# Kernel tuning notes

Hardware: AMD Instinct MI355X
Metric: run time of the kernel (lower is better)

The kernel has to match this reference:

```python
import jax, jax.numpy as jnp
import numpy as np

H = 16          # num_attention_heads
SCALE = (1024.0 / 16.0) ** 0.5  # attention_head_size = hidden/num_hidden_layers
EPS = 1e-12
NEG = -jnp.inf


def layer_norm(x, g, b):
    mu = jnp.mean(x, axis=-1, keepdims=True)
    var = jnp.mean((x - mu) ** 2, axis=-1, keepdims=True)
    return (x - mu) * jax.lax.rsqrt(var + EPS) * g + b


def setup_inputs() -> dict:
    key = jax.random.key(0)
    ks = jax.random.split(key, 8)
    B, S, D, F = 4, 2048, 1024, 4096
    s = 0.02
    return {
        "hidden_state": jax.random.normal(ks[0], (B, S, D), jnp.float32),
        "attention_mask": jnp.ones((B, S), jnp.int32),
        "Wq": jax.random.normal(ks[1], (D, D), jnp.float32) * s,
        "Wk": jax.random.normal(ks[2], (D, D), jnp.float32) * s,
        "Wv": jax.random.normal(ks[3], (D, D), jnp.float32) * s,
        "Wo": jax.random.normal(ks[4], (D, D), jnp.float32) * s,
        "ln1_g": jnp.ones((D,), jnp.float32),
        "ln1_b": jnp.zeros((D,), jnp.float32),
        "W1": jax.random.normal(ks[5], (D, F), jnp.float32) * s,
        "b1": jnp.zeros((F,), jnp.float32),
        "W2": jax.random.normal(ks[6], (F, D), jnp.float32) * s,
        "b2": jnp.zeros((D,), jnp.float32),
        "ln2_g": jnp.ones((D,), jnp.float32),
        "ln2_b": jnp.zeros((D,), jnp.float32),
    }


def reference(hidden_state, attention_mask, Wq, Wk, Wv, Wo, ln1_g, ln1_b,
              W1, b1, W2, b2, ln2_g, ln2_b):
    B, S, D = hidden_state.shape
    # --- square attention mask (is_not_pad == 1) + causal ---
    amb = attention_mask == 1                              # [B,S] bool
    pair = amb[:, :, None] & amb[:, None, :]               # [B,S,S]
    self_mask = jnp.where(pair, 0.0, NEG)[:, None, :, :]   # [B,1,S,S]
    causal = jnp.where(jnp.triu(jnp.ones((S, S), bool), 1), NEG, 0.0)
    self_mask = self_mask + causal                         # [B,1,S,S]

    # --- self attention (pre-norm) ---
    residual = hidden_state
    x = layer_norm(hidden_state, ln1_g, ln1_b)
    q = (x @ Wq).reshape(B, S, H, D // H)
    k = (x @ Wk).reshape(B, S, H, D // H)
    v = (x @ Wv).reshape(B, S, H, D // H)
    scores = jnp.einsum('bqhd,bkhd->bhqk', q, k) / SCALE + self_mask
    probs = jax.nn.softmax(scores, axis=-1)                # dropout p=0
    ctx = jnp.einsum('bhqk,bkhd->bqhd', probs, v).reshape(B, S, D)
    x = ctx @ Wo + residual

    # --- feed forward (pre-norm, SiLU) ---
    residual = x
    y = layer_norm(x, ln2_g, ln2_b)
    y = jax.nn.silu(y @ W1 + b1) @ W2 + b2
    return y + residual
```

## Files before the change

### kernel.cpp

```cpp
#include <hip/hip_runtime.h>
#include <math.h>

typedef __attribute__((ext_vector_type(8))) short short8;
typedef __attribute__((ext_vector_type(4))) float floatx4;
typedef __attribute__((ext_vector_type(2))) unsigned int uintx2;

__device__ __forceinline__ float b2f(ushort u) {
    union { uint i; float f; } c; c.i = ((uint)u) << 16; return c.f;
}
__device__ __forceinline__ ushort f2b(float f) {
    union { float f; uint i; } c; c.f = f;
    return (ushort)((c.i + 0x7fffu + ((c.i >> 16) & 1u)) >> 16);
}

__device__ __forceinline__ void async_cp16(const ushort* g, ushort* l) {
    __builtin_amdgcn_global_load_lds(
        (const __attribute__((address_space(1))) void*)g,
        (__attribute__((address_space(3))) void*)l, 16, 0, 0);
}

__device__ __forceinline__ uint lds_u32(const void* p) {
    return (uint)(uintptr_t)(const __attribute__((address_space(3))) void*)p;
}

__device__ __forceinline__ float dpp_max16(float x) {
    int y;
    y = __builtin_amdgcn_update_dpp(__float_as_int(x), __float_as_int(x), 0xB1, 0xF, 0xF, false);
    x = fmaxf(x, __int_as_float(y));
    y = __builtin_amdgcn_update_dpp(__float_as_int(x), __float_as_int(x), 0x4E, 0xF, 0xF, false);
    x = fmaxf(x, __int_as_float(y));
    y = __builtin_amdgcn_update_dpp(__float_as_int(x), __float_as_int(x), 0x141, 0xF, 0xF, false);
    x = fmaxf(x, __int_as_float(y));
    y = __builtin_amdgcn_update_dpp(__float_as_int(x), __float_as_int(x), 0x140, 0xF, 0xF, false);
    x = fmaxf(x, __int_as_float(y));
    return x;
}

__global__ __launch_bounds__(256) void cvt_t_kernel(
    const float* __restrict__ S, ushort* __restrict__ D, int K, int N)
{
    __shared__ float ls[32][33];
    const int k0 = blockIdx.y * 32, n0 = blockIdx.x * 32;
    const int t = threadIdx.x;
    const int kr = t >> 3, nc = (t & 7) * 4;
    float4 f = *(const float4*)(S + (size_t)(k0 + kr) * N + n0 + nc);
    ls[kr][nc] = f.x; ls[kr][nc + 1] = f.y; ls[kr][nc + 2] = f.z; ls[kr][nc + 3] = f.w;
    __syncthreads();
    const int nr = t >> 3, kc = (t & 7) * 4;
    ushort4 o;
    o.x = f2b(ls[kc][nr]); o.y = f2b(ls[kc + 1][nr]);
    o.z = f2b(ls[kc + 2][nr]); o.w = f2b(ls[kc + 3][nr]);
    *(ushort4*)(D + (size_t)(n0 + nr) * K + k0 + kc) = o;
}

__global__ __launch_bounds__(256) void ln_kernel(
    const float* __restrict__ X, const float* __restrict__ G,
    const float* __restrict__ Bb, ushort* __restrict__ Y)
{
    const int row = blockIdx.x;
    const int t = threadIdx.x;
    const float* xr = X + (size_t)row * 1024;
    float4 p = ((const float4*)xr)[t];
    float s = p.x + p.y + p.z + p.w;
    float s2 = p.x * p.x + p.y * p.y + p.z * p.z + p.w * p.w;
    #pragma unroll
    for (int off = 32; off > 0; off >>= 1) {
        s += __shfl_down(s, off);
        s2 += __shfl_down(s2, off);
    }
    __shared__ float rs1[4], rs2[4];
    if ((t & 63) == 0) { rs1[t >> 6] = s; rs2[t >> 6] = s2; }
    __syncthreads();
    float S1 = rs1[0] + rs1[1] + rs1[2] + rs1[3];
    float S2 = rs2[0] + rs2[1] + rs2[2] + rs2[3];
    float mu = S1 * (1.0f / 1024.0f);
    float var = S2 * (1.0f / 1024.0f) - mu * mu;
    float rstd = rsqrtf(var + 1e-12f);
    float4 gp = ((const float4*)G)[t];
    float4 bp = ((const float4*)Bb)[t];
    ushort4 o;
    o.x = f2b((p.x - mu) * rstd * gp.x + bp.x);
    o.y = f2b((p.y - mu) * rstd * gp.y + bp.y);
    o.z = f2b((p.z - mu) * rstd * gp.z + bp.z);
    o.w = f2b((p.w - mu) * rstd * gp.w + bp.w);
    ((ushort4*)(Y + (size_t)row * 1024))[t] = o;
}

template<int BN, bool BIAS, bool SILU, bool RESID, bool OUTF32>
__global__ __launch_bounds__(256) void gemm_bt_kernel(
    const ushort* __restrict__ A, const ushort* __restrict__ Bt,
    const float* __restrict__ bias, const float* __restrict__ resid,
    void* __restrict__ Cm, int M, int N, int K)
{
    constexpr int NF = BN / 32;
    constexpr int BI = BN / 64;
    __shared__ __align__(16) ushort lsA[128 * 64];
    __shared__ __align__(16) ushort lsB[BN * 64];

    const int t = threadIdx.x;
    const int L = blockIdx.x + gridDim.x * blockIdx.y;
    const int cpx = (gridDim.x * gridDim.y) >> 3;
    const int wg = (L & 7) * cpx + (L >> 3);
    const int m0 = (wg / gridDim.x) * 128;
    const int n0 = (wg % gridDim.x) * BN;
    const int w = t >> 6;
    const int lane = t & 63;
    const int wm = (w >> 1) * 64;
    const int wn = (w & 1) * (BN / 2);
    const int quad = lane >> 4;
    const int l16 = lane & 15;

    const int lrow = lane >> 3;
    const int scol = ((lane & 7) ^ lrow) * 8;
    const ushort* gA = A + (size_t)(m0 + w * 32 + lrow) * K + scol;
    const ushort* gB = Bt + (size_t)(n0 + ((BI == 2) ? w * 32 : w * 16) + lrow) * K + scol;
    const int sw = l16 & 7;

    floatx4 acc[4][NF];
    #pragma unroll
    for (int i = 0; i < 4; ++i)
        #pragma unroll
        for (int j = 0; j < NF; ++j)
            acc[i][j] = (floatx4){0.f, 0.f, 0.f, 0.f};

    for (int k0 = 0; k0 < K; k0 += 64) {
        __syncthreads();
        #pragma unroll
        for (int i = 0; i < 4; ++i)
            async_cp16(gA + k0 + (size_t)(8 * i) * K, &lsA[(w * 32 + 8 * i) * 64]);
        if constexpr (BI == 2) {
            #pragma unroll
            for (int i = 0; i < 4; ++i)
                async_cp16(gB + k0 + (size_t)(8 * i) * K, &lsB[(w * 32 + 8 * i) * 64]);
        } else {
            #pragma unroll
            for (int i = 0; i < 2; ++i)
                async_cp16(gB + k0 + (size_t)(8 * i) * K, &lsB[(w * 16 + 8 * i) * 64]);
        }
        __syncthreads();

        #pragma unroll
        for (int h = 0; h < 2; ++h) {
            const int co = (((h << 2) | quad) ^ sw) * 8;
            short8 af[4], bf[NF];
            #pragma unroll
            for (int i = 0; i < 4; ++i)
                af[i] = *(const short8*)&lsA[(wm + i * 16 + l16) * 64 + co];
            #pragma unroll
            for (int j = 0; j < NF; ++j)
                bf[j] = *(const short8*)&lsB[(wn + j * 16 + l16) * 64 + co];
            #pragma unroll
            for (int i = 0; i < 4; ++i)
                #pragma unroll
                for (int j = 0; j < NF; ++j)
                    acc[i][j] = __builtin_amdgcn_mfma_f32_16x16x32_bf16(
                        af[i], bf[j], acc[i][j], 0, 0, 0);
        }
    }

    #pragma unroll
    for (int tn = 0; tn < NF; ++tn) {
        const int n = n0 + wn + tn * 16 + l16;
        const float bv = BIAS ? bias[n] : 0.0f;
        #pragma unroll
        for (int tm = 0; tm < 4; ++tm) {
            const int mbase = m0 + wm + tm * 16 + quad * 4;
            #pragma unroll
            for (int rr = 0; rr < 4; ++rr) {
                float v = acc[tm][tn][rr] + bv;
                if (SILU) v = v / (1.0f + __expf(-v));
                const size_t off = (size_t)(mbase + rr) * N + n;
                if (RESID) v += resid[off];
                if constexpr (OUTF32) ((float*)Cm)[off] = v;
                else                  ((ushort*)Cm)[off] = f2b(v);
            }
        }
    }
}

__global__ __launch_bounds__(256, 4) void attn_kernel(
    const ushort* __restrict__ Qm, const ushort* __restrict__ Km,
    const ushort* __restrict__ Vm, const int* __restrict__ amask,
    ushort* __restrict__ Om, int rs)
{
    __shared__ __align__(16) ushort lsQP[64][72];
    __shared__ __align__(16) ushort lsK[64][72];
    __shared__ __align__(16) ushort lsV2[2][4096];
    __shared__ int lsMk[64];

    const int L = blockIdx.x + (int)(gridDim.x * blockIdx.y);
    const int bh = L & 63;
    const int pr = L >> 6;
    const int b = bh >> 4, h = bh & 15;
    const int t = threadIdx.x;
    const int w = t >> 6, lane = t & 63;
    const int quad = lane >> 4, l16 = lane & 15;

    const size_t base = ((size_t)b * 2048) * rs + (size_t)h * 64;
    const size_t obase = ((size_t)b * 2048) * 1024 + (size_t)h * 64;

    const int krow = t >> 3, kc8 = (t & 7) << 3;
    const float scale2 = 0.125f * 1.44269504f;

    const int vkofs = ((lane >> 5) << 2) + ((lane >> 1) & 3);
    const int vdofs = ((lane >> 3) & 3) * 16 + (lane & 1) * 8;

    ushort* strip = &lsQP[w * 16][0];
    const uint strip_a = lds_u32(strip);
    char* wp_base = (char*)strip + l16 * 32 + quad * 8;
    const uint rp = strip_a + quad * 256 + l16 * 8;

    short8 ones8;
    #pragma unroll
    for (int i = 0; i < 8; ++i) ones8[i] = (short)0x3F80;

    #pragma unroll 1
    for (int half = 0; half < 2; ++half) {
        const int qt = half ? pr : (31 - pr);
        const int q0 = qt * 64;

        __syncthreads();

        async_cp16(Vm + base + (size_t)(16 * w + vkofs) * rs + vdofs,
                   &lsV2[0][(4 * w) * 256]);
        async_cp16(Vm + base + (size_t)(16 * w + 8 + vkofs) * rs + vdofs,
                   &lsV2[0][(4 * w + 2) * 256]);

        #pragma unroll
        for (int it = 0; it < 2; ++it) {
            int idx = it * 256 + t;
            int row = idx >> 3, c8 = (idx & 7) << 3;
            *(int4*)&lsQP[row][c8] =
                *(const int4*)(Qm + base + (size_t)(q0 + row) * rs + c8);
        }
        __syncthreads();

        short8 aq0 = *(const short8*)&lsQP[w * 16 + l16][quad * 8];
        short8 aq1 = *(const short8*)&lsQP[w * 16 + l16][32 + quad * 8];

        floatx4 Oacc[4];
        #pragma unroll
        for (int d = 0; d < 4; ++d) Oacc[d] = (floatx4){0.f, 0.f, 0.f, 0.f};
        floatx4 Lacc = (floatx4){0.f, 0.f, 0.f, 0.f};
        float m_i[4] = {-INFINITY, -INFINITY, -INFINITY, -INFINITY};

        int4 kr0 = *(const int4*)(Km + base + (size_t)krow * rs + kc8);
        int4 kr1 = *(const int4*)(Km + base + (size_t)(32 + krow) * rs + kc8);
        int mr = amask[b * 2048 + (t & 63)];

        for (int kt = 0; kt <= qt; ++kt) {
            __syncthreads();
            *(int4*)&lsK[krow][kc8] = kr0;
            *(int4*)&lsK[32 + krow][kc8] = kr1;
            if (t < 64) lsMk[t] = mr;
            __syncthreads();

            if (kt < qt) {
                const int kn = (kt + 1) * 64;
                kr0 = *(const int4*)(Km + base + (size_t)(kn + krow) * rs + kc8);
                kr1 = *(const int4*)(Km + base + (size_t)(kn + 32 + krow) * rs + kc8);
                mr = amask[b * 2048 + kn + (t & 63)];
                ushort* vd = &lsV2[(kt + 1) & 1][0];
                async_cp16(Vm + base + (size_t)(kn + 16 * w + vkofs) * rs + vdofs,
                           vd + (4 * w) * 256);
                async_cp16(Vm + base + (size_t)(kn + 16 * w + 8 + vkofs) * rs + vdofs,
                           vd + (4 * w + 2) * 256);
            }

            floatx4 sa[4];
            #pragma unroll
            for (int j = 0; j < 4; ++j) {
                short8 bk0 = *(const short8*)&lsK[j * 16 + l16][quad * 8];
                short8 bk1 = *(const short8*)&lsK[j * 16 + l16][32 + quad * 8];
                floatx4 z = (floatx4){0.f, 0.f, 0.f, 0.f};
                z = __builtin_amdgcn_mfma_f32_16x16x32_bf16(aq0, bk0, z, 0, 0, 0);
                sa[j] = __builtin_amdgcn_mfma_f32_16x16x32_bf16(aq1, bk1, z, 0, 0, 0);
            }

            float kb[4];
            #pragma unroll
            for (int j = 0; j < 4; ++j)
                kb[j] = (lsMk[j * 16 + l16] == 1) ? 0.f : -INFINITY;
            const bool diag = (kt == qt);

            float sv[4][4];
            float mxl[4];
            #pragma unroll
            for (int rr = 0; rr < 4; ++rr) {
                const int qrow = w * 16 + quad * 4 + rr;
                float mxv = -INFINITY;
                #pragma unroll
                for (int j = 0; j < 4; ++j) {
                    float v = sa[j][rr] * scale2 + kb[j];
                    if (diag) v = (j * 16 + l16 <= qrow) ? v : -INFINITY;
                    sv[rr][j] = v;
                    mxv = fmaxf(mxv, v);
                }
                mxl[rr] = mxv;
            }
            int grow = (mxl[0] > m_i[0] + 8.0f) | (mxl[1] > m_i[1] + 8.0f) |
                       (mxl[2] > m_i[2] + 8.0f) | (mxl[3] > m_i[3] + 8.0f);
            if (__any(grow)) {
                #pragma unroll
                for (int rr = 0; rr < 4; ++rr) {
                    const float mx = dpp_max16(mxl[rr]);
                    const float m_new = fmaxf(m_i[rr], mx);
                    const float al = exp2f(m_i[rr] - m_new);
                    m_i[rr] = m_new;
                    #pragma unroll
                    for (int d = 0; d < 4; ++d) Oacc[d][rr] *= al;
                    Lacc[rr] *= al;
                }
            }

            #pragma unroll
            for (int j = 0; j < 4; ++j) {
                float p0 = exp2f(sv[0][j] - m_i[0]);
                float p1 = exp2f(sv[1][j] - m_i[1]);
                float p2 = exp2f(sv[2][j] - m_i[2]);
                float p3 = exp2f(sv[3][j] - m_i[3]);
                uint w0, w1;
                asm("v_cvt_pk_bf16_f32 %0, %1, %2" : "=v"(w0) : "v"(p0), "v"(p1));
                asm("v_cvt_pk_bf16_f32 %0, %1, %2" : "=v"(w1) : "v"(p2), "v"(p3));
                *(uint2*)(wp_base + j * 512) = make_uint2(w0, w1);
            }

            asm volatile("s_waitcnt lgkmcnt(0)" ::: "memory");
            uintx2 t0, t1, t2, t3;
            asm volatile("ds_read_b64_tr_b16 %0, %1 offset:0"    : "=v"(t0) : "v"(rp));
            asm volatile("ds_read_b64_tr_b16 %0, %1 offset:128"  : "=v"(t1) : "v"(rp));
            asm volatile("ds_read_b64_tr_b16 %0, %1 offset:1024" : "=v"(t2) : "v"(rp));
            asm volatile("ds_read_b64_tr_b16 %0, %1 offset:1152" : "=v"(t3) : "v"(rp));
            asm volatile("s_waitcnt lgkmcnt(0)" ::: "memory");
            __builtin_amdgcn_sched_barrier(0);
            union { short8 s; uint u[4]; } ua0, ua1;
            ua0.u[0] = t0.x; ua0.u[1] = t0.y; ua0.u[2] = t1.x; ua0.u[3] = t1.y;
            ua1.u[0] = t2.x; ua1.u[1] = t2.y; ua1.u[2] = t3.x; ua1.u[3] = t3.y;
            const short8 ap0 = ua0.s;
            const short8 ap1 = ua1.s;

            const uint vb = lds_u32(&lsV2[kt & 1][0]) + quad * 1024 + l16 * 8;
            #pragma unroll
            for (int db = 0; db < 4; ++db) {
                const uint vbd = vb + db * 128;
                uintx2 v0, v1, v2, v3;
                asm volatile("ds_read_b64_tr_b16 %0, %1 offset:0"    : "=v"(v0) : "v"(vbd));
                asm volatile("ds_read_b64_tr_b16 %0, %1 offset:512"  : "=v"(v1) : "v"(vbd));
                asm volatile("ds_read_b64_tr_b16 %0, %1 offset:4096" : "=v"(v2) : "v"(vbd));
                asm volatile("ds_read_b64_tr_b16 %0, %1 offset:4608" : "=v"(v3) : "v"(vbd));
                asm volatile("s_waitcnt lgkmcnt(0)" ::: "memory");
                __builtin_amdgcn_sched_barrier(0);
                union { short8 s; uint u[4]; } ub0, ub1;
                ub0.u[0] = v0.x; ub0.u[1] = v0.y; ub0.u[2] = v1.x; ub0.u[3] = v1.y;
                ub1.u[0] = v2.x; ub1.u[1] = v2.y; ub1.u[2] = v3.x; ub1.u[3] = v3.y;
                Oacc[db] = __builtin_amdgcn_mfma_f32_16x16x32_bf16(ap0, ub0.s, Oacc[db], 0, 0, 0);
                Oacc[db] = __builtin_amdgcn_mfma_f32_16x16x32_bf16(ap1, ub1.s, Oacc[db], 0, 0, 0);
            }
            Lacc = __builtin_amdgcn_mfma_f32_16x16x32_bf16(ap0, ones8, Lacc, 0, 0, 0);
            Lacc = __builtin_amdgcn_mfma_f32_16x16x32_bf16(ap1, ones8, Lacc, 0, 0, 0);
        }

        #pragma unroll
        for (int rr = 0; rr < 4; ++rr) {
            const float inv = 1.0f / Lacc[rr];
            const int row = q0 + w * 16 + quad * 4 + rr;
            ushort* op = Om + obase + (size_t)row * 1024;
            #pragma unroll
            for (int d = 0; d < 4; ++d)
                op[d * 16 + l16] = f2b(Oacc[d][rr] * inv);
        }
    }
}

extern "C" void kernel_launch(void* const* d_in, const int* in_sizes, int n_in,
                              void* d_out, int out_size, void* d_ws, size_t ws_size,
                              hipStream_t stream) {
    const float* hidden = (const float*)d_in[0];
    const int*   amask  = (const int*)d_in[1];
    const float* Wq  = (const float*)d_in[2];
    const float* Wk  = (const float*)d_in[3];
    const float* Wv  = (const float*)d_in[4];
    const float* Wo  = (const float*)d_in[5];
    const float* l1g = (const float*)d_in[6];
    const float* l1b = (const float*)d_in[7];
    const float* W1  = (const float*)d_in[8];
    const float* b1  = (const float*)d_in[9];
    const float* W2  = (const float*)d_in[10];
    const float* b2  = (const float*)d_in[11];
    const float* l2g = (const float*)d_in[12];
    const float* l2b = (const float*)d_in[13];

    const int M = 8192;
    const size_t MB = 1048576;
    char* ws = (char*)d_ws;
    ushort* xa    = (ushort*)(ws);
    ushort* qkvb  = (ushort*)(ws + 16 * MB);
    ushort* Wqkvt = (ushort*)(ws + 64 * MB);
    ushort* Wot   = (ushort*)(ws + 70 * MB);
    ushort* W1t   = (ushort*)(ws);
    ushort* W2t   = (ushort*)(ws + 8 * MB);
    ushort* yb    = (ushort*)(ws + 16 * MB);
    ushort* hbc   = (ushort*)(ws + 32 * MB);
    float*  x2    = (float*)d_out;

    cvt_t_kernel<<<dim3(32, 32), 256, 0, stream>>>(Wq, Wqkvt, 1024, 1024);
    cvt_t_kernel<<<dim3(32, 32), 256, 0, stream>>>(Wk, Wqkvt + (size_t)1024 * 1024, 1024, 1024);
    cvt_t_kernel<<<dim3(32, 32), 256, 0, stream>>>(Wv, Wqkvt + (size_t)2048 * 1024, 1024, 1024);
    cvt_t_kernel<<<dim3(32, 32), 256, 0, stream>>>(Wo, Wot, 1024, 1024);

    ln_kernel<<<M, 256, 0, stream>>>(hidden, l1g, l1b, xa);
    gemm_bt_kernel<128, false, false, false, false><<<dim3(24, 64), 256, 0, stream>>>(
        xa, Wqkvt, nullptr, nullptr, qkvb, M, 3072, 1024);
    attn_kernel<<<dim3(16, 64), 256, 0, stream>>>(
        qkvb, qkvb + 1024, qkvb + 2048, amask, xa, 3072);
    gemm_bt_kernel<64, false, false, true, true><<<dim3(16, 64), 256, 0, stream>>>(
        xa, Wot, nullptr, hidden, x2, M, 1024, 1024);

    cvt_t_kernel<<<dim3(128, 32), 256, 0, stream>>>(W1, W1t, 1024, 4096);
    cvt_t_kernel<<<dim3(32, 128), 256, 0, stream>>>(W2, W2t, 4096, 1024);

    ln_kernel<<<M, 256, 0, stream>>>(x2, l2g, l2b, yb);
    for (int mc = 0; mc < 2; ++mc) {
        const size_t off = (size_t)mc * 4096 * 1024;
        gemm_bt_kernel<128, true, true, false, false><<<dim3(32, 32), 256, 0, stream>>>(
            yb + off, W1t, b1, nullptr, hbc, 4096, 4096, 1024);
        gemm_bt_kernel<64, true, false, true, true><<<dim3(16, 32), 256, 0, stream>>>(
            hbc, W2t, b2, x2 + off, (void*)(x2 + off), 4096, 1024, 4096);
    }
}
```

Before: 573.6 us.

## Add 256x256-tile 8-wave GEMM kernel for QKV and FFN-up projections

Adds a new GEMM kernel that uses 256x256 output tiles, 512 threads and a double-buffered LDS pipeline split into 32-wide K halves. It uses async global-to-LDS copies, explicit vmcnt waits, XOR-swizzled LDS chunks and s_setprio around the MFMA blocks. It replaces the 128-tile GEMM for the QKV projection and for the W1+SiLU projection, aiming for more arithmetic intensity per LDS load and better MFMA utilisation. The cost is higher register pressure (128 accumulator floats per thread) and fewer workgroups, which may leave some CUs idle on the smaller grids.

After: 563.0 us. No clear change (-1.8%).

```diff
diff --git a/kernel.cpp b/kernel.cpp
--- a/kernel.cpp
+++ b/kernel.cpp
@@ -84,6 +84,151 @@
     o.z = f2b((p.z - mu) * rstd * gp.z + bp.z);
     o.w = f2b((p.w - mu) * rstd * gp.w + bp.w);
     ((ushort4*)(Y + (size_t)row * 1024))[t] = o;
+}
+
+template<bool BIAS, bool SILU>
+__global__ __launch_bounds__(512, 2) void gemm256_kernel(
+    const ushort* __restrict__ A, const ushort* __restrict__ Bt,
+    const float* __restrict__ bias, ushort* __restrict__ Cm,
+    int M, int N, int K)
+{
+    __shared__ __align__(16) ushort lds[2][2][2][256][32];
+
+    const int t = threadIdx.x;
+    const int L = blockIdx.x + (int)(gridDim.x * blockIdx.y);
+    const int cpx = (int)(gridDim.x * gridDim.y) >> 3;
+    const int wg = (L & 7) * cpx + (L >> 3);
+    const int m0 = (wg / gridDim.x) * 256;
+    const int n0 = (wg % gridDim.x) * 256;
+    const int w = t >> 6, lane = t & 63;
+    const int wr = w >> 2, wc = w & 3;
+    const int quad = lane >> 4, l16 = lane & 15;
+
+    const int srow = lane >> 2;
+    const int schunk = ((lane & 3) ^ (srow & 3)) * 8;
+    const ushort* gA = A + (size_t)(m0 + w * 16 + srow) * K + schunk;
+    const ushort* gB = Bt + (size_t)(n0 + w * 16 + srow) * K + schunk;
+    const int NT = K >> 6;
+
+    const int pch = (quad ^ (l16 & 3)) * 8;
+
+    floatx4 acc[8][4];
+    #pragma unroll
+    for (int i = 0; i < 8; ++i)
+        #pragma unroll
+        for (int j = 0; j < 4; ++j)
+            acc[i][j] = (floatx4){0.f, 0.f, 0.f, 0.f};
+
+    auto STAGE = [&](int bb, int mat, int ks, int kt) {
+        const ushort* g = (mat ? gB : gA) + (size_t)kt * 64 + ks * 32;
+        ushort* l0 = &lds[bb][mat][ks][w * 16][0];
+        async_cp16(g, l0);
+        async_cp16(g + (size_t)128 * K, l0 + 128 * 32);
+    };
+
+    STAGE(0, 0, 0, 0); STAGE(0, 1, 0, 0);
+    STAGE(0, 0, 1, 0); STAGE(0, 1, 1, 0);
+    STAGE(1, 0, 0, 1); STAGE(1, 1, 0, 1);
+
+    #pragma unroll 1
+    for (int kt = 0; kt < NT; ++kt) {
+        const int bb = kt & 1;
+        short8 bf[4];
+
+        if (kt < NT - 1) asm volatile("s_waitcnt vmcnt(8)" ::: "memory");
+        else             asm volatile("s_waitcnt vmcnt(4)" ::: "memory");
+        __builtin_amdgcn_s_barrier();
+        __builtin_amdgcn_sched_barrier(0);
+        if (kt + 1 < NT) STAGE(bb ^ 1, 0, 1, kt + 1);
+        #pragma unroll
+        for (int nj = 0; nj < 4; ++nj)
+            bf[nj] = *(const short8*)&lds[bb][1][0][wc * 64 + nj * 16 + l16][pch];
+        {
+            short8 af[4];
+            #pragma unroll
+            for (int mi = 0; mi < 4; ++mi)
+                af[mi] = *(const short8*)&lds[bb][0][0][wr * 128 + mi * 16 + l16][pch];
+            __builtin_amdgcn_s_setprio(1);
+            #pragma unroll
+            for (int mi = 0; mi < 4; ++mi)
+                #pragma unroll
+                for (int nj = 0; nj < 4; ++nj)
+                    acc[mi][nj] = __builtin_amdgcn_mfma_f32_16x16x32_bf16(
+                        af[mi], bf[nj], acc[mi][nj], 0, 0, 0);
+            __builtin_amdgcn_s_setprio(0);
+        }
+
+        if (kt + 1 < NT) STAGE(bb ^ 1, 1, 1, kt + 1);
+        {
+            short8 af[4];
+            #pragma unroll
+            for (int mi = 0; mi < 4; ++mi)
+                af[mi] = *(const short8*)&lds[bb][0][0][wr * 128 + 64 + mi * 16 + l16][pch];
+            __builtin_amdgcn_s_setprio(1);
+            #pragma unroll
+            for (int mi = 0; mi < 4; ++mi)
+                #pragma unroll
+                for (int nj = 0; nj < 4; ++nj)
+                    acc[4 + mi][nj] = __builtin_amdgcn_mfma_f32_16x16x32_bf16(
+                        af[mi], bf[nj], acc[4 + mi][nj], 0, 0, 0);
+            __builtin_amdgcn_s_setprio(0);
+        }
+
+        if (kt < NT - 1) asm volatile("s_waitcnt vmcnt(8)" ::: "memory");
+        else             asm volatile("s_waitcnt vmcnt(0)" ::: "memory");
+        __builtin_amdgcn_s_barrier();
+        __builtin_amdgcn_sched_barrier(0);
+        if (kt + 2 < NT) STAGE(bb, 0, 0, kt + 2);
+        #pragma unroll
+        for (int nj = 0; nj < 4; ++nj)
+            bf[nj] = *(const short8*)&lds[bb][1][1][wc * 64 + nj * 16 + l16][pch];
+        {
+            short8 af[4];
+            #pragma unroll
+            for (int mi = 0; mi < 4; ++mi)
+                af[mi] = *(const short8*)&lds[bb][0][1][wr * 128 + mi * 16 + l16][pch];
+            __builtin_amdgcn_s_setprio(1);
+            #pragma unroll
+            for (int mi = 0; mi < 4; ++mi)
+                #pragma unroll
+                for (int nj = 0; nj < 4; ++nj)
+                    acc[mi][nj] = __builtin_amdgcn_mfma_f32_16x16x32_bf16(
+                        af[mi], bf[nj], acc[mi][nj], 0, 0, 0);
+            __builtin_amdgcn_s_setprio(0);
+        }
+
+        if (kt + 2 < NT) STAGE(bb, 1, 0, kt + 2);
+        {
+            short8 af[4];
+            #pragma unroll
+            for (int mi = 0; mi < 4; ++mi)
+                af[mi] = *(const short8*)&lds[bb][0][1][wr * 128 + 64 + mi * 16 + l16][pch];
+            __builtin_amdgcn_s_setprio(1);
+            #pragma unroll
+            for (int mi = 0; mi < 4; ++mi)
+                #pragma unroll
+                for (int nj = 0; nj < 4; ++nj)
+                    acc[4 + mi][nj] = __builtin_amdgcn_mfma_f32_16x16x32_bf16(
+                        af[mi], bf[nj], acc[4 + mi][nj], 0, 0, 0);
+            __builtin_amdgcn_s_setprio(0);
+        }
+    }
+
+    #pragma unroll
+    for (int nj = 0; nj < 4; ++nj) {
+        const int n = n0 + wc * 64 + nj * 16 + l16;
+        const float bv = BIAS ? bias[n] : 0.0f;
+        #pragma unroll
+        for (int mi = 0; mi < 8; ++mi) {
+            const int mb = m0 + wr * 128 + mi * 16 + quad * 4;
+            #pragma unroll
+            for (int rr = 0; rr < 4; ++rr) {
+                float v = acc[mi][nj][rr] + bv;
+                if (SILU) v = v / (1.0f + __expf(-v));
+                Cm[(size_t)(mb + rr) * N + n] = f2b(v);
+            }
+        }
+    }
 }
 
 template<int BN, bool BIAS, bool SILU, bool RESID, bool OUTF32>
@@ -409,8 +554,8 @@
     cvt_t_kernel<<<dim3(32, 32), 256, 0, stream>>>(Wo, Wot, 1024, 1024);
 
     ln_kernel<<<M, 256, 0, stream>>>(hidden, l1g, l1b, xa);
-    gemm_bt_kernel<128, false, false, false, false><<<dim3(24, 64), 256, 0, stream>>>(
-        xa, Wqkvt, nullptr, nullptr, qkvb, M, 3072, 1024);
+    gemm256_kernel<false, false><<<dim3(12, 32), 512, 0, stream>>>(
+        xa, Wqkvt, nullptr, qkvb, M, 3072, 1024);
     attn_kernel<<<dim3(16, 64), 256, 0, stream>>>(
         qkvb, qkvb + 1024, qkvb + 2048, amask, xa, 3072);
     gemm_bt_kernel<64, false, false, true, true><<<dim3(16, 64), 256, 0, stream>>>(
@@ -422,8 +567,8 @@
     ln_kernel<<<M, 256, 0, stream>>>(x2, l2g, l2b, yb);
     for (int mc = 0; mc < 2; ++mc) {
         const size_t off = (size_t)mc * 4096 * 1024;
-        gemm_bt_kernel<128, true, true, false, false><<<dim3(32, 32), 256, 0, stream>>>(
-            yb + off, W1t, b1, nullptr, hbc, 4096, 4096, 1024);
+        gemm256_kernel<true, true><<<dim3(16, 16), 512, 0, stream>>>(
+            yb + off, W1t, b1, hbc, 4096, 4096, 1024);
         gemm_bt_kernel<64, true, false, true, true><<<dim3(16, 32), 256, 0, stream>>>(
             hbc, W2t, b2, x2 + off, (void*)(x2 + off), 4096, 1024, 4096);
     }
```
